# Optimization experiments

Hardware: AMD Instinct MI355X
Metric: run time of the kernel (lower is better)

Reference implementation:

```python
import jax, jax.numpy as jnp
import numpy as np

N_NODES = 50000
N_EDGES = 800000
N_GRAPHS = 8
D_IN, D_HID, D_OUT = 128, 128, 64


def setup_inputs() -> dict:
    key = jax.random.key(0)
    ks = jax.random.split(key, 8)
    x = jax.random.normal(ks[0], (N_NODES, D_IN), jnp.float32)
    src = jax.random.randint(ks[1], (N_EDGES,), 0, N_NODES, dtype=jnp.int32)
    dst = jax.random.randint(ks[2], (N_EDGES,), 0, N_NODES, dtype=jnp.int32)
    graph_id = jnp.sort(jax.random.randint(ks[3], (N_NODES,), 0, N_GRAPHS, dtype=jnp.int32))
    s1 = 1.0 / np.sqrt(D_IN)
    s2 = 1.0 / np.sqrt(D_HID)
    W1 = jax.random.normal(ks[4], (D_IN, D_HID), jnp.float32) * s1
    b1 = jnp.zeros((D_HID,), jnp.float32)
    W2 = jax.random.normal(ks[5], (D_HID, D_HID), jnp.float32) * s2
    b2 = jnp.zeros((D_HID,), jnp.float32)
    Wl = jax.random.normal(ks[6], (D_HID, D_OUT), jnp.float32) * s2
    bl = jnp.zeros((D_OUT,), jnp.float32)
    return dict(x=x, W1=W1, b1=b1, W2=W2, b2=b2, Wl=Wl, bl=bl,
                src=src, dst=dst, graph_id=graph_id)


def _graph_conv(x, W, b, src, dst):
    # DGL GraphConv, norm='both': h' = D_in^{-1/2} A (D_out^{-1/2} x W) + b
    n = x.shape[0]
    ones = jnp.ones((src.shape[0],), x.dtype)
    out_deg = jax.ops.segment_sum(ones, src, num_segments=n)
    in_deg = jax.ops.segment_sum(ones, dst, num_segments=n)
    norm_src = jax.lax.rsqrt(jnp.clip(out_deg, 1.0))  # [N]
    norm_dst = jax.lax.rsqrt(jnp.clip(in_deg, 1.0))   # [N]
    h = (x * norm_src[:, None]) @ W                    # [N, D]
    agg = jax.ops.segment_sum(h[src], dst, num_segments=n)  # gather-scatter SpMM
    return agg * norm_dst[:, None] + b


def reference(x, W1, b1, W2, b2, Wl, bl, src, dst, graph_id):
    h = jax.nn.relu(_graph_conv(x, W1, b1, src, dst))
    h = _graph_conv(h, W2, b2, src, dst)
    # dgl.mean_nodes over batched graph: per-graph mean of node features
    cnt = jax.ops.segment_sum(jnp.ones((x.shape[0],), x.dtype), graph_id,
                              num_segments=N_GRAPHS)
    pooled = jax.ops.segment_sum(h, graph_id, num_segments=N_GRAPHS)
    means = pooled / jnp.clip(cnt, 1.0)[:, None]       # [B, D_HID]
    return means @ Wl + bl                              # [B, D_OUT]
```

## Files before the change

### kernel.cpp

```cpp
#include <hip/hip_runtime.h>
#include <hip/hip_bf16.h>

#define N_NODES 50000
#define N_EDGES 800000
#define N_GRAPHS 8
#define MAXDEG 64
#define NRANGE 4
#define NCHUNK 64
#define RSZ (N_NODES / NRANGE)
#define CHE (N_EDGES / NCHUNK)
#define SENT_ROW 65535

typedef __attribute__((ext_vector_type(8))) short short8;
typedef __attribute__((ext_vector_type(4))) float floatx4;
typedef __attribute__((ext_vector_type(2))) float floatx2;

static __device__ __forceinline__ ushort f2b(float f) {
    union { float f; unsigned u; } v; v.f = f;
    return (ushort)((v.u + 0x7FFF + ((v.u >> 16) & 1)) >> 16);
}
static __device__ __forceinline__ float b2f(unsigned u) {
    union { unsigned u; float f; } v; v.u = u << 16;
    return v.f;
}
static __device__ __forceinline__ unsigned char f2q(float f) {
    int p = __builtin_amdgcn_cvt_pk_fp8_f32(f, f, 0, false);
    return (unsigned char)(p & 0xff);
}

__global__ __launch_bounds__(1024) void prep_kernel(
    const int* __restrict__ src, const int* __restrict__ dst,
    const float* __restrict__ W1, const float* __restrict__ W2,
    const int* __restrict__ gid,
    ushort* __restrict__ counts_in, ushort* __restrict__ counts_out,
    ushort* __restrict__ Wt1, ushort* __restrict__ Wt2,
    int* __restrict__ start,
    unsigned char* __restrict__ hA, uint4* __restrict__ slot_fill)
{
    int b = blockIdx.x, t = threadIdx.x;
    if (b < 256) {
        __shared__ unsigned h[RSZ];
        int c = b & (NCHUNK - 1), r = b >> 6;
        int lo = r * RSZ;
        for (int j = t; j < RSZ; j += 1024) h[j] = 0;
        __syncthreads();
        int ebeg = c * CHE, eend = ebeg + CHE;
        for (int i = ebeg + t; i < eend; i += 1024) {
            int s = src[i], d = dst[i];
            unsigned ds = (unsigned)(d - lo);
            if (ds < RSZ) atomicAdd(&h[ds >> 1], 1u << ((ds & 1) * 16));
            unsigned ss = (unsigned)(s - lo);
            if (ss < RSZ) atomicAdd(&h[(RSZ / 2) + (ss >> 1)], 1u << ((ss & 1) * 16));
        }
        __syncthreads();
        unsigned* ci = (unsigned*)(counts_in  + (size_t)c * N_NODES + lo);
        unsigned* co = (unsigned*)(counts_out + (size_t)c * N_NODES + lo);
        for (int j = t; j < RSZ / 2; j += 1024) {
            ci[j] = h[j];
            co[j] = h[(RSZ / 2) + j];
        }
    } else if (b < 272) {
        int i = (b - 256) * 1024 + t;
        int c = i >> 7, k = i & 127;
        Wt1[i] = f2b(W1[k * 128 + c]);
        Wt2[i] = f2b(W2[k * 128 + c]);
        if (b == 256 && t < 32)
            ((unsigned*)(hA + (size_t)SENT_ROW * 128))[t] = 0u;
    } else if (b < 321) {
        int i = (b - 272) * 1024 + t;
        if (i < N_NODES) {
            int g = gid[i];
            int gp = (i == 0) ? -1 : gid[i - 1];
            for (int k = gp + 1; k <= g; ++k) start[k] = i;
            if (i == N_NODES - 1)
                for (int k = g + 1; k <= N_GRAPHS; ++k) start[k] = N_NODES;
        }
    } else {
        int i = (b - 321) * 1024 + t;
        if (i < (N_NODES * MAXDEG * 2) / 16)
            slot_fill[i] = make_uint4(0xFFFFFFFFu, 0xFFFFFFFFu, 0xFFFFFFFFu, 0xFFFFFFFFu);
    }
}

__global__ __launch_bounds__(256) void scan_kernel(
    const ushort* __restrict__ counts_in, const ushort* __restrict__ counts_out,
    ushort* __restrict__ base, int* __restrict__ in_deg,
    float* __restrict__ ns, float* __restrict__ nd)
{
    int v = blockIdx.x * 256 + threadIdx.x;
    if (v >= N_NODES) return;
    unsigned od = 0;
    #pragma unroll 8
    for (int c = 0; c < NCHUNK; ++c) od += counts_out[(size_t)c * N_NODES + v];
    unsigned run = 0;
    #pragma unroll 8
    for (int c = 0; c < NCHUNK; ++c) {
        base[(size_t)c * N_NODES + v] = (ushort)run;
        run += counts_in[(size_t)c * N_NODES + v];
    }
    in_deg[v] = (int)run;
    ns[v] = rsqrtf(fmaxf((float)od, 1.f));
    nd[v] = rsqrtf(fmaxf((float)run, 1.f));
}

__global__ __launch_bounds__(1024) void scatter_kernel(
    const int* __restrict__ src, const int* __restrict__ dst,
    const ushort* __restrict__ base, ushort* __restrict__ slot)
{
    __shared__ unsigned h[RSZ / 2];
    int t = threadIdx.x;
    int c = blockIdx.x & (NCHUNK - 1), r = blockIdx.x >> 6;
    int lo = r * RSZ;
    const unsigned* bp = (const unsigned*)(base + (size_t)c * N_NODES + lo);
    for (int j = t; j < RSZ / 2; j += 1024) h[j] = bp[j];
    __syncthreads();
    int ebeg = c * CHE, eend = ebeg + CHE;
    for (int i = ebeg + t; i < eend; i += 1024) {
        int d = dst[i];
        unsigned ds = (unsigned)(d - lo);
        if (ds < RSZ) {
            int sh = (ds & 1) * 16;
            unsigned old = atomicAdd(&h[ds >> 1], 1u << sh);
            unsigned pos = (old >> sh) & 0xffff;
            if (pos < MAXDEG) slot[(size_t)d * MAXDEG + pos] = (ushort)src[i];
        }
    }
}

template<int FP32_IN>
__global__ __launch_bounds__(256, 2) void mfma_gemm_kernel(
    const void* __restrict__ Xv, const float* __restrict__ scale,
    const ushort* __restrict__ Wt, unsigned char* __restrict__ Y)
{
    int t = threadIdx.x;
    int wv = t >> 6, lane = t & 63;
    int m = lane & 15, q = lane >> 4;
    int tile = blockIdx.x * 4 + wv;
    if (tile >= (N_NODES >> 4)) return;

    short8 B[8][4];
    #pragma unroll
    for (int cb = 0; cb < 8; ++cb)
        #pragma unroll
        for (int kb = 0; kb < 4; ++kb)
            B[cb][kb] = *(const short8*)&Wt[(size_t)(cb * 16 + m) * 128 + kb * 32 + q * 8];

    int row = tile * 16 + m;
    short8 a[4];
    if (FP32_IN) {
        const float* X = (const float*)Xv;
        float s = scale[row];
        #pragma unroll
        for (int kb = 0; kb < 4; ++kb) {
            const float* p = X + (size_t)row * 128 + kb * 32 + q * 8;
            float4 f0 = *(const float4*)p;
            float4 f1 = *(const float4*)(p + 4);
            short8 av;
            av[0] = (short)f2b(f0.x * s); av[1] = (short)f2b(f0.y * s);
            av[2] = (short)f2b(f0.z * s); av[3] = (short)f2b(f0.w * s);
            av[4] = (short)f2b(f1.x * s); av[5] = (short)f2b(f1.y * s);
            av[6] = (short)f2b(f1.z * s); av[7] = (short)f2b(f1.w * s);
            a[kb] = av;
        }
    } else {
        const ushort* X = (const ushort*)Xv;
        #pragma unroll
        for (int kb = 0; kb < 4; ++kb)
            a[kb] = *(const short8*)(X + (size_t)row * 128 + kb * 32 + q * 8);
    }
    floatx4 acc[8] = {};
    #pragma unroll
    for (int cb = 0; cb < 8; ++cb)
        #pragma unroll
        for (int kb = 0; kb < 4; ++kb)
            acc[cb] = __builtin_amdgcn_mfma_f32_16x16x32_bf16(B[cb][kb], a[kb], acc[cb], 0, 0, 0);

    unsigned char* yr = Y + (size_t)row * 128;
    #pragma unroll
    for (int cb = 0; cb < 8; ++cb) {
        int lo = __builtin_amdgcn_cvt_pk_fp8_f32(acc[cb][0], acc[cb][1], 0, false);
        int pk = __builtin_amdgcn_cvt_pk_fp8_f32(acc[cb][2], acc[cb][3], lo, true);
        *(unsigned*)(yr + cb * 16 + q * 4) = (unsigned)pk;
    }
}

__global__ __launch_bounds__(256) void spmm_fp8_kernel(
    const unsigned char* __restrict__ H, const int* __restrict__ in_deg,
    const ushort* __restrict__ slot, const float* __restrict__ norm_dst,
    const float* __restrict__ norm_src, const float* __restrict__ bias,
    ushort* __restrict__ Y, int relu_scale)
{
    int w = (blockIdx.x * blockDim.x + threadIdx.x) >> 6;
    int lane = threadIdx.x & 63;
    if (w >= N_NODES) return;
    int cnt = min(in_deg[w], MAXDEG);
    const ushort* lst = slot + (size_t)w * MAXDEG;
    int g = lane >> 4;
    int c8 = (lane & 15) * 8;
    int myslot = lst[lane];
    float acc[8] = {};
    for (int e = 0; e < cnt; e += 8) {
        int s0 = __shfl(myslot, e + g, 64);
        int s1 = __shfl(myslot, e + 4 + g, 64);
        uint2 v0 = *(const uint2*)&H[(size_t)s0 * 128 + c8];
        uint2 v1 = *(const uint2*)&H[(size_t)s1 * 128 + c8];
        floatx2 a01 = __builtin_amdgcn_cvt_pk_f32_fp8((int)v0.x, false);
        floatx2 a23 = __builtin_amdgcn_cvt_pk_f32_fp8((int)v0.x, true);
        floatx2 a45 = __builtin_amdgcn_cvt_pk_f32_fp8((int)v0.y, false);
        floatx2 a67 = __builtin_amdgcn_cvt_pk_f32_fp8((int)v0.y, true);
        floatx2 b01 = __builtin_amdgcn_cvt_pk_f32_fp8((int)v1.x, false);
        floatx2 b23 = __builtin_amdgcn_cvt_pk_f32_fp8((int)v1.x, true);
        floatx2 b45 = __builtin_amdgcn_cvt_pk_f32_fp8((int)v1.y, false);
        floatx2 b67 = __builtin_amdgcn_cvt_pk_f32_fp8((int)v1.y, true);
        acc[0] += a01.x + b01.x; acc[1] += a01.y + b01.y;
        acc[2] += a23.x + b23.x; acc[3] += a23.y + b23.y;
        acc[4] += a45.x + b45.x; acc[5] += a45.y + b45.y;
        acc[6] += a67.x + b67.x; acc[7] += a67.y + b67.y;
    }
    #pragma unroll
    for (int j = 0; j < 8; ++j) {
        acc[j] += __shfl_xor(acc[j], 16, 64);
        acc[j] += __shfl_xor(acc[j], 32, 64);
    }
    float ndv = norm_dst[w];
    float4 b0 = *(const float4*)&bias[c8];
    float4 b1 = *(const float4*)&bias[c8 + 4];
    float r[8];
    r[0] = acc[0] * ndv + b0.x; r[1] = acc[1] * ndv + b0.y;
    r[2] = acc[2] * ndv + b0.z; r[3] = acc[3] * ndv + b0.w;
    r[4] = acc[4] * ndv + b1.x; r[5] = acc[5] * ndv + b1.y;
    r[6] = acc[6] * ndv + b1.z; r[7] = acc[7] * ndv + b1.w;
    if (relu_scale) {
        float nsv = norm_src[w];
        #pragma unroll
        for (int j = 0; j < 8; ++j) r[j] = fmaxf(r[j], 0.f) * nsv;
    }
    if (lane < 16) {
        uint4 o;
        o.x = (unsigned)f2b(r[0]) | ((unsigned)f2b(r[1]) << 16);
        o.y = (unsigned)f2b(r[2]) | ((unsigned)f2b(r[3]) << 16);
        o.z = (unsigned)f2b(r[4]) | ((unsigned)f2b(r[5]) << 16);
        o.w = (unsigned)f2b(r[6]) | ((unsigned)f2b(r[7]) << 16);
        *(uint4*)&Y[(size_t)w * 128 + c8] = o;
    }
}

__global__ __launch_bounds__(256) void pool_kernel(
    const ushort* __restrict__ H, const int* __restrict__ start,
    float* __restrict__ part)
{
    __shared__ float red[128];
    int t = threadIdx.x;
    int g = blockIdx.x >> 5, j = blockIdx.x & 31;
    int beg0 = start[g], len = start[g + 1] - beg0;
    int sbeg = beg0 + (int)(((long long)len * j) >> 5);
    int send = beg0 + (int)(((long long)len * (j + 1)) >> 5);
    int wv = t >> 6, lane = t & 63;
    int rg = lane >> 4;
    int c8 = (lane & 15) * 8;
    float acc[8] = {};
    for (int v = sbeg + wv * 4 + rg; v < send; v += 16) {
        uint4 u = *(const uint4*)&H[(size_t)v * 128 + c8];
        acc[0] += b2f(u.x & 0xffff); acc[1] += b2f(u.x >> 16);
        acc[2] += b2f(u.y & 0xffff); acc[3] += b2f(u.y >> 16);
        acc[4] += b2f(u.z & 0xffff); acc[5] += b2f(u.z >> 16);
        acc[6] += b2f(u.w & 0xffff); acc[7] += b2f(u.w >> 16);
    }
    #pragma unroll
    for (int k = 0; k < 8; ++k) {
        acc[k] += __shfl_xor(acc[k], 16, 64);
        acc[k] += __shfl_xor(acc[k], 32, 64);
    }
    if (t < 128) red[t] = 0.f;
    __syncthreads();
    if (lane < 16) {
        #pragma unroll
        for (int k = 0; k < 8; ++k) atomicAdd(&red[c8 + k], acc[k]);
    }
    __syncthreads();
    if (t < 128) part[(size_t)blockIdx.x * 128 + t] = red[t];
}

__global__ __launch_bounds__(512) void head_kernel(
    const float* __restrict__ part, const int* __restrict__ start,
    const float* __restrict__ Wl, const float* __restrict__ bl,
    float* __restrict__ out)
{
    __shared__ float means[N_GRAPHS * 128];
    int t = threadIdx.x;
    for (int i = t; i < N_GRAPHS * 128; i += 512) {
        int g = i >> 7, k = i & 127;
        float s = 0.f;
        #pragma unroll 8
        for (int j = 0; j < 32; ++j) s += part[(size_t)(g * 32 + j) * 128 + k];
        float cnt = (float)(start[g + 1] - start[g]);
        means[i] = s / fmaxf(cnt, 1.f);
    }
    __syncthreads();
    int g = t >> 6, c = t & 63;
    float acc = bl[c];
    #pragma unroll 8
    for (int k = 0; k < 128; ++k)
        acc = fmaf(means[g * 128 + k], Wl[k * 64 + c], acc);
    out[g * 64 + c] = acc;
}

extern "C" void kernel_launch(void* const* d_in, const int* in_sizes, int n_in,
                              void* d_out, int out_size, void* d_ws, size_t ws_size,
                              hipStream_t stream) {
    const float* x   = (const float*)d_in[0];
    const float* W1  = (const float*)d_in[1];
    const float* b1  = (const float*)d_in[2];
    const float* W2  = (const float*)d_in[3];
    const float* b2  = (const float*)d_in[4];
    const float* Wl  = (const float*)d_in[5];
    const float* bl  = (const float*)d_in[6];
    const int*   src = (const int*)d_in[7];
    const int*   dst = (const int*)d_in[8];
    const int*   gid = (const int*)d_in[9];

    const int n = N_NODES;

    char* ws = (char*)d_ws;
    size_t off = 0;
    auto alloc = [&](size_t bytes) { size_t o = off; off += (bytes + 255) & ~(size_t)255; return o; };
    unsigned char* hA = (unsigned char*)(ws + alloc((size_t)65536 * 128));
    ushort* hB        = (ushort*)(ws + alloc((size_t)n * 128 * 2));
    ushort* slot      = (ushort*)(ws + alloc((size_t)n * MAXDEG * 2));
    ushort* counts_in = (ushort*)(ws + alloc((size_t)NCHUNK * n * 2));
    ushort* counts_out= (ushort*)(ws + alloc((size_t)NCHUNK * n * 2));
    ushort* basev     = (ushort*)(ws + alloc((size_t)NCHUNK * n * 2));
    float* norm_src   = (float*) (ws + alloc((size_t)n * 4));
    float* norm_dst   = (float*) (ws + alloc((size_t)n * 4));
    int*   in_deg     = (int*)   (ws + alloc((size_t)n * 4));
    int*   startb     = (int*)   (ws + alloc((size_t)(N_GRAPHS + 1) * 4));
    ushort* Wt1       = (ushort*)(ws + alloc((size_t)128 * 128 * 2));
    ushort* Wt2       = (ushort*)(ws + alloc((size_t)128 * 128 * 2));
    float* part       = (float*) (ws + alloc((size_t)N_GRAPHS * 32 * 128 * 4));

    int spmm_blocks = (n + 3) / 4;
    int gemm_blocks = ((n >> 4) + 3) / 4;
    int fill_blocks = ((N_NODES * MAXDEG * 2) / 16 + 1023) / 1024;

    prep_kernel<<<321 + fill_blocks, 1024, 0, stream>>>(
        src, dst, W1, W2, gid, counts_in, counts_out, Wt1, Wt2, startb,
        hA, (uint4*)slot);
    scan_kernel<<<(n + 255) / 256, 256, 0, stream>>>(counts_in, counts_out, basev,
                                                     in_deg, norm_src, norm_dst);
    scatter_kernel<<<NRANGE * NCHUNK, 1024, 0, stream>>>(src, dst, basev, slot);
    mfma_gemm_kernel<1><<<gemm_blocks, 256, 0, stream>>>(x, norm_src, Wt1, hA);
    spmm_fp8_kernel<<<spmm_blocks, 256, 0, stream>>>(hA, in_deg, slot, norm_dst,
                                                     norm_src, b1, hB, 1);
    mfma_gemm_kernel<0><<<gemm_blocks, 256, 0, stream>>>(hB, nullptr, Wt2, hA);
    spmm_fp8_kernel<<<spmm_blocks, 256, 0, stream>>>(hA, in_deg, slot, norm_dst,
                                                     nullptr, b2, hB, 0);
    pool_kernel<<<N_GRAPHS * 32, 256, 0, stream>>>(hB, startb, part);
    head_kernel<<<1, 512, 0, stream>>>(part, startb, Wl, bl, (float*)d_out);
}
```

Before: 218.6 us.

## Split fp8 feature matrix into two column planes and run SpMM per plane

The GEMM now writes its fp8 output as two 64-column planes, each 64 bytes per row, instead of one 128-byte row. Each SpMM is launched twice, once per plane, so the gathered working set per pass is halved and fits better in cache. Within a pass, 8 lanes cover a row and 8 neighbour rows are gathered per step, with up to 64 neighbour loads issued before any accumulation. The sentinel row moves to index 50000, and both SpMM passes per layer reread the slot lists and degrees in exchange for the smaller gather footprint.

```diff
diff --git a/kernel.cpp b/kernel.cpp
--- a/kernel.cpp
+++ b/kernel.cpp
@@ -9,7 +9,9 @@
 #define NCHUNK 64
 #define RSZ (N_NODES / NRANGE)
 #define CHE (N_EDGES / NCHUNK)
-#define SENT_ROW 65535
+#define SENT 50000
+#define PLANE_ROWS 50048
+#define PLANE_BYTES ((size_t)PLANE_ROWS * 64)
 
 typedef __attribute__((ext_vector_type(8))) short short8;
 typedef __attribute__((ext_vector_type(4))) float floatx4;
@@ -22,10 +24,6 @@
 static __device__ __forceinline__ float b2f(unsigned u) {
     union { unsigned u; float f; } v; v.u = u << 16;
     return v.f;
-}
-static __device__ __forceinline__ unsigned char f2q(float f) {
-    int p = __builtin_amdgcn_cvt_pk_fp8_f32(f, f, 0, false);
-    return (unsigned char)(p & 0xff);
 }
 
 __global__ __launch_bounds__(1024) void prep_kernel(
@@ -64,8 +62,12 @@
         int c = i >> 7, k = i & 127;
         Wt1[i] = f2b(W1[k * 128 + c]);
         Wt2[i] = f2b(W2[k * 128 + c]);
-        if (b == 256 && t < 32)
-            ((unsigned*)(hA + (size_t)SENT_ROW * 128))[t] = 0u;
+        if (b == 256) {
+            if (t < 16)
+                ((unsigned*)(hA + (size_t)SENT * 64))[t] = 0u;
+            else if (t < 32)
+                ((unsigned*)(hA + PLANE_BYTES + (size_t)SENT * 64))[t - 16] = 0u;
+        }
     } else if (b < 321) {
         int i = (b - 272) * 1024 + t;
         if (i < N_NODES) {
@@ -78,7 +80,7 @@
     } else {
         int i = (b - 321) * 1024 + t;
         if (i < (N_NODES * MAXDEG * 2) / 16)
-            slot_fill[i] = make_uint4(0xFFFFFFFFu, 0xFFFFFFFFu, 0xFFFFFFFFu, 0xFFFFFFFFu);
+            slot_fill[i] = make_uint4(0xC350C350u, 0xC350C350u, 0xC350C350u, 0xC350C350u);
     }
 }
 
@@ -175,56 +177,62 @@
         for (int kb = 0; kb < 4; ++kb)
             acc[cb] = __builtin_amdgcn_mfma_f32_16x16x32_bf16(B[cb][kb], a[kb], acc[cb], 0, 0, 0);
 
-    unsigned char* yr = Y + (size_t)row * 128;
+    unsigned char* p0 = Y + (size_t)row * 64;
+    unsigned char* p1 = Y + PLANE_BYTES + (size_t)row * 64;
     #pragma unroll
     for (int cb = 0; cb < 8; ++cb) {
         int lo = __builtin_amdgcn_cvt_pk_fp8_f32(acc[cb][0], acc[cb][1], 0, false);
         int pk = __builtin_amdgcn_cvt_pk_fp8_f32(acc[cb][2], acc[cb][3], lo, true);
-        *(unsigned*)(yr + cb * 16 + q * 4) = (unsigned)pk;
+        unsigned char* yp = (cb < 4) ? p0 : p1;
+        *(unsigned*)(yp + (cb & 3) * 16 + q * 4) = (unsigned)pk;
     }
 }
 
 __global__ __launch_bounds__(256) void spmm_fp8_kernel(
-    const unsigned char* __restrict__ H, const int* __restrict__ in_deg,
+    const unsigned char* __restrict__ Hp, const int* __restrict__ in_deg,
     const ushort* __restrict__ slot, const float* __restrict__ norm_dst,
     const float* __restrict__ norm_src, const float* __restrict__ bias,
-    ushort* __restrict__ Y, int relu_scale)
+    ushort* __restrict__ Y, int colbase, int relu_scale)
 {
     int w = (blockIdx.x * blockDim.x + threadIdx.x) >> 6;
     int lane = threadIdx.x & 63;
     if (w >= N_NODES) return;
     int cnt = min(in_deg[w], MAXDEG);
+    int jmax = (cnt + 7) >> 3;
     const ushort* lst = slot + (size_t)w * MAXDEG;
-    int g = lane >> 4;
-    int c8 = (lane & 15) * 8;
+    int rg = lane >> 3;
+    int c8 = (lane & 7) * 8;
     int myslot = lst[lane];
+    uint2 v[8];
+    #pragma unroll
+    for (int j = 0; j < 8; ++j)
+        if (j < jmax) {
+            int s = __shfl(myslot, j * 8 + rg, 64);
+            v[j] = *(const uint2*)&Hp[(size_t)s * 64 + c8];
+        }
     float acc[8] = {};
-    for (int e = 0; e < cnt; e += 8) {
-        int s0 = __shfl(myslot, e + g, 64);
-        int s1 = __shfl(myslot, e + 4 + g, 64);
-        uint2 v0 = *(const uint2*)&H[(size_t)s0 * 128 + c8];
-        uint2 v1 = *(const uint2*)&H[(size_t)s1 * 128 + c8];
-        floatx2 a01 = __builtin_amdgcn_cvt_pk_f32_fp8((int)v0.x, false);
-        floatx2 a23 = __builtin_amdgcn_cvt_pk_f32_fp8((int)v0.x, true);
-        floatx2 a45 = __builtin_amdgcn_cvt_pk_f32_fp8((int)v0.y, false);
-        floatx2 a67 = __builtin_amdgcn_cvt_pk_f32_fp8((int)v0.y, true);
-        floatx2 b01 = __builtin_amdgcn_cvt_pk_f32_fp8((int)v1.x, false);
-        floatx2 b23 = __builtin_amdgcn_cvt_pk_f32_fp8((int)v1.x, true);
-        floatx2 b45 = __builtin_amdgcn_cvt_pk_f32_fp8((int)v1.y, false);
-        floatx2 b67 = __builtin_amdgcn_cvt_pk_f32_fp8((int)v1.y, true);
-        acc[0] += a01.x + b01.x; acc[1] += a01.y + b01.y;
-        acc[2] += a23.x + b23.x; acc[3] += a23.y + b23.y;
-        acc[4] += a45.x + b45.x; acc[5] += a45.y + b45.y;
-        acc[6] += a67.x + b67.x; acc[7] += a67.y + b67.y;
-    }
+    #pragma unroll
+    for (int j = 0; j < 8; ++j)
+        if (j < jmax) {
+            floatx2 p01 = __builtin_amdgcn_cvt_pk_f32_fp8((int)v[j].x, false);
+            floatx2 p23 = __builtin_amdgcn_cvt_pk_f32_fp8((int)v[j].x, true);
+            floatx2 p45 = __builtin_amdgcn_cvt_pk_f32_fp8((int)v[j].y, false);
+            floatx2 p67 = __builtin_amdgcn_cvt_pk_f32_fp8((int)v[j].y, true);
+            acc[0] += p01.x; acc[1] += p01.y;
+            acc[2] += p23.x; acc[3] += p23.y;
+            acc[4] += p45.x; acc[5] += p45.y;
+            acc[6] += p67.x; acc[7] += p67.y;
+        }
     #pragma unroll
     for (int j = 0; j < 8; ++j) {
+        acc[j] += __shfl_xor(acc[j], 8, 64);
         acc[j] += __shfl_xor(acc[j], 16, 64);
         acc[j] += __shfl_xor(acc[j], 32, 64);
     }
     float ndv = norm_dst[w];
-    float4 b0 = *(const float4*)&bias[c8];
-    float4 b1 = *(const float4*)&bias[c8 + 4];
+    int col = colbase + c8;
+    float4 b0 = *(const float4*)&bias[col];
+    float4 b1 = *(const float4*)&bias[col + 4];
     float r[8];
     r[0] = acc[0] * ndv + b0.x; r[1] = acc[1] * ndv + b0.y;
     r[2] = acc[2] * ndv + b0.z; r[3] = acc[3] * ndv + b0.w;
@@ -235,13 +243,13 @@
         #pragma unroll
         for (int j = 0; j < 8; ++j) r[j] = fmaxf(r[j], 0.f) * nsv;
     }
-    if (lane < 16) {
+    if (lane < 8) {
         uint4 o;
         o.x = (unsigned)f2b(r[0]) | ((unsigned)f2b(r[1]) << 16);
         o.y = (unsigned)f2b(r[2]) | ((unsigned)f2b(r[3]) << 16);
         o.z = (unsigned)f2b(r[4]) | ((unsigned)f2b(r[5]) << 16);
         o.w = (unsigned)f2b(r[6]) | ((unsigned)f2b(r[7]) << 16);
-        *(uint4*)&Y[(size_t)w * 128 + c8] = o;
+        *(uint4*)&Y[(size_t)w * 128 + col] = o;
     }
 }
 
@@ -324,7 +332,7 @@
     char* ws = (char*)d_ws;
     size_t off = 0;
     auto alloc = [&](size_t bytes) { size_t o = off; off += (bytes + 255) & ~(size_t)255; return o; };
-    unsigned char* hA = (unsigned char*)(ws + alloc((size_t)65536 * 128));
+    unsigned char* hA = (unsigned char*)(ws + alloc(2 * PLANE_BYTES));
     ushort* hB        = (ushort*)(ws + alloc((size_t)n * 128 * 2));
     ushort* slot      = (ushort*)(ws + alloc((size_t)n * MAXDEG * 2));
     ushort* counts_in = (ushort*)(ws + alloc((size_t)NCHUNK * n * 2));
@@ -338,6 +346,9 @@
     ushort* Wt2       = (ushort*)(ws + alloc((size_t)128 * 128 * 2));
     float* part       = (float*) (ws + alloc((size_t)N_GRAPHS * 32 * 128 * 4));
 
+    const unsigned char* plane0 = hA;
+    const unsigned char* plane1 = hA + PLANE_BYTES;
+
     int spmm_blocks = (n + 3) / 4;
     int gemm_blocks = ((n >> 4) + 3) / 4;
     int fill_blocks = ((N_NODES * MAXDEG * 2) / 16 + 1023) / 1024;
@@ -349,11 +360,15 @@
                                                      in_deg, norm_src, norm_dst);
     scatter_kernel<<<NRANGE * NCHUNK, 1024, 0, stream>>>(src, dst, basev, slot);
     mfma_gemm_kernel<1><<<gemm_blocks, 256, 0, stream>>>(x, norm_src, Wt1, hA);
-    spmm_fp8_kernel<<<spmm_blocks, 256, 0, stream>>>(hA, in_deg, slot, norm_dst,
-                                                     norm_src, b1, hB, 1);
+    spmm_fp8_kernel<<<spmm_blocks, 256, 0, stream>>>(plane0, in_deg, slot, norm_dst,
+                                                     norm_src, b1, hB, 0, 1);
+    spmm_fp8_kernel<<<spmm_blocks, 256, 0, stream>>>(plane1, in_deg, slot, norm_dst,
+                                                     norm_src, b1, hB, 64, 1);
     mfma_gemm_kernel<0><<<gemm_blocks, 256, 0, stream>>>(hB, nullptr, Wt2, hA);
-    spmm_fp8_kernel<<<spmm_blocks, 256, 0, stream>>>(hA, in_deg, slot, norm_dst,
-                                                     nullptr, b2, hB, 0);
+    spmm_fp8_kernel<<<spmm_blocks, 256, 0, stream>>>(plane0, in_deg, slot, norm_dst,
+                                                     nullptr, b2, hB, 0, 0);
+    spmm_fp8_kernel<<<spmm_blocks, 256, 0, stream>>>(plane1, in_deg, slot, norm_dst,
+                                                     nullptr, b2, hB, 64, 0);
     pool_kernel<<<N_GRAPHS * 32, 256, 0, stream>>>(hB, startb, part);
     head_kernel<<<1, 512, 0, stream>>>(part, startb, Wl, bl, (float*)d_out);
 }
```

After: 248.6 us. +13.7%, slower.
